# Performance work log

Hardware: AMD Instinct MI355X
Metric: run time of the kernel (lower is better)

The kernel has to match this reference:

```python
import jax, jax.numpy as jnp
import numpy as np

N = 100000
E = 1600000
IN_C = 128
HID = 32
HEADS = 4
OUT_C = 16
G = 128
NEG_SLOPE = 0.2


def setup_inputs() -> dict:
    key = jax.random.key(0)
    ks = jax.random.split(key, 16)
    x = jax.random.normal(ks[0], (N, IN_C), dtype=jnp.float32)
    edge_index = jax.random.randint(ks[1], (2, E), 0, N, dtype=jnp.int64)
    batch = jnp.sort(jax.random.randint(ks[2], (N,), 0, G, dtype=jnp.int64))
    node_weights = jax.random.uniform(ks[3], (N, 1), dtype=jnp.float32)
    s = 1.0 / np.sqrt(IN_C)
    W1 = jax.random.uniform(ks[4], (IN_C, HEADS * HID), jnp.float32, -s, s)
    att_src1 = jax.random.uniform(ks[5], (HEADS, HID), jnp.float32, -s, s)
    att_dst1 = jax.random.uniform(ks[6], (HEADS, HID), jnp.float32, -s, s)
    b1 = jnp.zeros((HEADS * HID,), jnp.float32)
    s2 = 1.0 / np.sqrt(HEADS * HID)
    W2 = jax.random.uniform(ks[7], (HEADS * HID, HID), jnp.float32, -s2, s2)
    att_src2 = jax.random.uniform(ks[8], (1, HID), jnp.float32, -s2, s2)
    att_dst2 = jax.random.uniform(ks[9], (1, HID), jnp.float32, -s2, s2)
    b2 = jnp.zeros((HID,), jnp.float32)
    s3 = 1.0 / np.sqrt(HID)
    fcW = jax.random.uniform(ks[10], (HID, OUT_C), jnp.float32, -s3, s3)
    fcb = jax.random.uniform(ks[11], (OUT_C,), jnp.float32, -s3, s3)
    return {"x": x, "edge_index": edge_index, "batch": batch,
            "node_weights": node_weights,
            "W1": W1, "att_src1": att_src1, "att_dst1": att_dst1, "b1": b1,
            "W2": W2, "att_src2": att_src2, "att_dst2": att_dst2, "b2": b2,
            "fcW": fcW, "fcb": fcb}


def gat_conv(x, src, dst, W, att_src, att_dst, bias, heads, ch, concat):
    n = x.shape[0]
    h = (x @ W).reshape(n, heads, ch)                       # [N,H,C]
    a_src = jnp.sum(h * att_src[None], axis=-1)             # [N,H]
    a_dst = jnp.sum(h * att_dst[None], axis=-1)             # [N,H]
    e = jax.nn.leaky_relu(a_src[src] + a_dst[dst], NEG_SLOPE)  # [E,H]
    # segment softmax over incoming edges of each destination node
    e_max = jax.ops.segment_max(e, dst, num_segments=n)
    ex = jnp.exp(e - e_max[dst])
    denom = jax.ops.segment_sum(ex, dst, num_segments=n)
    alpha = ex / denom[dst]                                 # [E,H]
    msg = h[src] * alpha[..., None]                         # [E,H,C]
    out = jax.ops.segment_sum(msg, dst, num_segments=n)     # [N,H,C]
    if concat:
        out = out.reshape(n, heads * ch)
    else:
        out = out.mean(axis=1)
    return out + bias


def reference(x, edge_index, batch, node_weights,
              W1, att_src1, att_dst1, b1,
              W2, att_src2, att_dst2, b2,
              fcW, fcb):
    n = x.shape[0]
    # PyG GATConv adds self-loops by default
    loop = jnp.arange(n, dtype=edge_index.dtype)
    src = jnp.concatenate([edge_index[0], loop])
    dst = jnp.concatenate([edge_index[1], loop])

    h = x * node_weights
    h = jax.nn.elu(gat_conv(h, src, dst, W1, att_src1, att_dst1, b1, HEADS, HID, True))
    h = jax.nn.elu(gat_conv(h, src, dst, W2, att_src2, att_dst2, b2, 1, HID, False))
    # global mean pool over graphs
    sums = jax.ops.segment_sum(h, batch, num_segments=G)
    cnts = jax.ops.segment_sum(jnp.ones((n,), h.dtype), batch, num_segments=G)
    pooled = sums / jnp.maximum(cnts, 1.0)[:, None]
    return pooled @ fcW + fcb
```

## Files before the change

### kernel.cpp

```cpp
#include <hip/hip_runtime.h>
#include <cstdint>

#define NGRAPH 128
#define NEG 0.2f
#define NB_MAX 512
#define BSH 8
#define BSZ 256
#define CAP 8192
#define RC  6144

typedef unsigned int uint;
typedef unsigned short ushort;
typedef unsigned char uchar;
typedef __attribute__((ext_vector_type(8))) short bf16x8;
typedef __attribute__((ext_vector_type(4))) float f32x4;
typedef __attribute__((ext_vector_type(2))) float f32x2;

union U4B { uint4 u; bf16x8 v; };

__device__ __forceinline__ ushort f2bf(float f) {
  uint u = __float_as_uint(f);
  uint r = (u + 0x7FFF + ((u >> 16) & 1)) >> 16;
  return (ushort)r;
}

__device__ __forceinline__ uint cvtpkbf16(float lo, float hi) {
  uint r;
  asm("v_cvt_pk_bf16_f32 %0, %1, %2" : "=v"(r) : "v"(lo), "v"(hi));
  return r;
}

__device__ __forceinline__ void pkfma(f32x2& acc, f32x2 f, f32x2 w) {
  asm("v_pk_fma_f32 %0, %1, %2, %0" : "+v"(acc) : "v"(f), "v"(w));
}

__device__ __forceinline__ float bperm_f(int addr, float v) {
  return __int_as_float(__builtin_amdgcn_ds_bpermute(addr, __float_as_int(v)));
}
__device__ __forceinline__ int bperm_i(int addr, int v) {
  return __builtin_amdgcn_ds_bpermute(addr, v);
}

__device__ __forceinline__ int wave_incl_scan_i(int v) {
  int lane = threadIdx.x & 63;
#pragma unroll
  for (int off = 1; off < 64; off <<= 1) {
    int u = __shfl_up(v, off, 64);
    if (lane >= off) v += u;
  }
  return v;
}

__global__ void k_bin(const int* __restrict__ ei,
                      const float* __restrict__ W1, const float* __restrict__ W2,
                      ushort* __restrict__ Wt1, ushort* __restrict__ Wt2,
                      int E, int Etot, int NB, int nbin,
                      int* __restrict__ bcur, uint* __restrict__ bbuf) {
  if (blockIdx.x >= (uint)nbin) {
    int t2 = (blockIdx.x - nbin) * 256 + threadIdx.x;
    if (t2 < 16384) {
      int n = t2 >> 7, k = t2 & 127;
      Wt1[t2] = f2bf(W1[k * 128 + n]);
    } else {
      int u = t2 - 16384;
      int n = u >> 7, k = u & 127;
      Wt2[u] = f2bf(W2[k * 32 + n]);
    }
    return;
  }
  __shared__ int h[NB_MAX];
  __shared__ int baseo[NB_MAX];
  __shared__ uint crec[4096];
  __shared__ ushort cbkt[4096];
  int t = threadIdx.x;
  for (int b = t; b < NB; b += 256) h[b] = 0;
  __syncthreads();
  int cbase = blockIdx.x * 4096;
  int cend = min(cbase + 4096, Etot);
  int nch = cend - cbase;
  for (int i = t; i < nch; i += 256) {
    int e = cbase + i;
    int s, d;
    if (e < E) { s = ei[e]; d = ei[E + e]; } else { s = e - E; d = s; }
    int b = d >> BSH;
    crec[i] = ((uint)(d & (BSZ - 1)) << 17) | (uint)s;
    cbkt[i] = (ushort)b;
    atomicAdd(&h[b], 1);
  }
  __syncthreads();
  for (int b = t; b < NB; b += 256) {
    int c = h[b];
    baseo[b] = c ? atomicAdd(&bcur[b], c) : 0;
    h[b] = 0;
  }
  __syncthreads();
  for (int i = t; i < nch; i += 256) {
    int b = cbkt[i];
    int r = atomicAdd(&h[b], 1);
    bbuf[(size_t)b * CAP + baseo[b] + r] = crec[i];
  }
}

__global__ void k_bg(const uint* __restrict__ bbuf, const int* __restrict__ bcur,
                     int NB, int N, int* __restrict__ offs, int* __restrict__ ssrc,
                     const float* __restrict__ x, const ushort* __restrict__ Wt,
                     const float* __restrict__ nw, const float* __restrict__ att_s,
                     const float* __restrict__ att_d, uchar* __restrict__ hb1,
                     float* __restrict__ asrc, float* __restrict__ adst) {
  __shared__ int sst[NB_MAX + 1];
  __shared__ int wsum2[4];
  __shared__ int deg[BSZ];
  __shared__ uint rcache[RC];
  if (blockIdx.x < (uint)NB) {
    int t = threadIdx.x, lane = t & 63, wid = t >> 6;
    int v0 = (2 * t < NB) ? bcur[2 * t] : 0;
    int v1 = (2 * t + 1 < NB) ? bcur[2 * t + 1] : 0;
    int s = v0 + v1;
    int sv = wave_incl_scan_i(s);
    if (lane == 63) wsum2[wid] = sv;
    deg[t] = 0;
    __syncthreads();
    if (t == 0) {
      int r = 0;
#pragma unroll
      for (int k = 0; k < 4; k++) { int x2 = wsum2[k]; wsum2[k] = r; r += x2; }
    }
    __syncthreads();
    int excl = wsum2[wid] + sv - s;
    sst[2 * t] = excl;
    sst[2 * t + 1] = excl + v0;
    if (t == 255) sst[512] = excl + v0 + v1;
    __syncthreads();
    int b = blockIdx.x;
    int ebeg = sst[b], eend = sst[b + 1];
    int cnt = eend - ebeg;
    const uint* brow = bbuf + (size_t)b * CAP;
    for (int i = t; i < cnt; i += BSZ) {
      uint rec = brow[i];
      if (i < RC) rcache[i] = rec;
      atomicAdd(&deg[rec >> 17], 1);
    }
    __syncthreads();
    int v = deg[t];
    int sv2 = wave_incl_scan_i(v);
    if (lane == 63) wsum2[wid] = sv2;
    __syncthreads();
    if (t == 0) {
      int r = 0;
#pragma unroll
      for (int k = 0; k < 4; k++) { int x2 = wsum2[k]; wsum2[k] = r; r += x2; }
    }
    __syncthreads();
    int excl2 = wsum2[wid] + sv2 - v;
    int node = (b << BSH) + t;
    if (node < N) offs[node] = ebeg + excl2;
    if (b == 0 && t == 0) offs[N] = sst[512];
    __syncthreads();
    deg[t] = excl2;
    __syncthreads();
    for (int i = t; i < cnt; i += BSZ) {
      uint rec = (i < RC) ? rcache[i] : brow[i];
      int r = atomicAdd(&deg[rec >> 17], 1);
      ssrc[ebeg + r] = (int)(rec & 0x1FFFF);
    }
    return;
  }
  int bid = blockIdx.x - NB;
  int wv = threadIdx.x >> 6, l = threadIdx.x & 63;
  int lg = l >> 4, lr = l & 15;
  int row0 = bid * 64 + wv * 16;
  int node = row0 + lr;
  bool valid = node < N;
  float sc = valid ? nw[node] : 0.f;
  bf16x8 xfr[4];
  const float* xr = x + (size_t)node * 128;
#pragma unroll
  for (int kc = 0; kc < 4; kc++) {
    float v[8];
    if (valid) {
      float4 q0 = *reinterpret_cast<const float4*>(xr + kc * 32 + lg * 8);
      float4 q1 = *reinterpret_cast<const float4*>(xr + kc * 32 + lg * 8 + 4);
      v[0] = q0.x; v[1] = q0.y; v[2] = q0.z; v[3] = q0.w;
      v[4] = q1.x; v[5] = q1.y; v[6] = q1.z; v[7] = q1.w;
    } else {
#pragma unroll
      for (int j = 0; j < 8; j++) v[j] = 0.f;
    }
    U4B a;
    a.u.x = cvtpkbf16(v[0] * sc, v[1] * sc);
    a.u.y = cvtpkbf16(v[2] * sc, v[3] * sc);
    a.u.z = cvtpkbf16(v[4] * sc, v[5] * sc);
    a.u.w = cvtpkbf16(v[6] * sc, v[7] * sc);
    xfr[kc] = a.v;
  }
  float pS[4] = {}, pD[4] = {};
#pragma unroll
  for (int ct = 0; ct < 8; ct++) {
    f32x4 acc = {0.f, 0.f, 0.f, 0.f};
    const ushort* wrow = Wt + (size_t)(ct * 16 + lr) * 128;
#pragma unroll
    for (int kc = 0; kc < 4; kc++) {
      U4B bfr;
      bfr.u = *reinterpret_cast<const uint4*>(wrow + kc * 32 + lg * 8);
      acc = __builtin_amdgcn_mfma_f32_16x16x32_bf16(bfr.v, xfr[kc], acc, 0, 0, 0);
    }
    int c0 = ct * 16 + lg * 4;
    if (valid) {
      uint u8 = (uint)__builtin_amdgcn_cvt_pk_fp8_f32(acc[0], acc[1], 0, false);
      u8 = (uint)__builtin_amdgcn_cvt_pk_fp8_f32(acc[2], acc[3], u8, true);
      *reinterpret_cast<uint*>(hb1 + (size_t)node * 128 + c0) = u8;
    }
    float4 as4 = *reinterpret_cast<const float4*>(att_s + c0);
    float4 ad4 = *reinterpret_cast<const float4*>(att_d + c0);
    int h = ct >> 1;
    pS[h] += acc[0] * as4.x + acc[1] * as4.y + acc[2] * as4.z + acc[3] * as4.w;
    pD[h] += acc[0] * ad4.x + acc[1] * ad4.y + acc[2] * ad4.z + acc[3] * ad4.w;
  }
#pragma unroll
  for (int off = 16; off < 64; off <<= 1) {
#pragma unroll
    for (int h = 0; h < 4; h++) {
      pS[h] += __shfl_xor(pS[h], off, 64);
      pD[h] += __shfl_xor(pD[h], off, 64);
    }
  }
  if (lg == 0 && valid) {
    *reinterpret_cast<float4*>(asrc + node * 4) = make_float4(pS[0], pS[1], pS[2], pS[3]);
    *reinterpret_cast<float4*>(adst + node * 4) = make_float4(pD[0], pD[1], pD[2], pD[3]);
  }
}

__global__ void k_aggr1(const int* __restrict__ offs, const int* __restrict__ ssrc,
                        const uchar* __restrict__ hb, const float* __restrict__ asrc,
                        const float* __restrict__ adst, const float* __restrict__ bias,
                        const ushort* __restrict__ Wt2, const float* __restrict__ as2,
                        const float* __restrict__ ad2, uchar* __restrict__ rec2,
                        float* __restrict__ adst2, int N) {
  __shared__ ushort rowl[4][136];
  int tid = threadIdx.x;
  int wv = tid >> 6, l = tid & 63;
  int d = blockIdx.x * 4 + wv;
  int dc = min(d, N - 1);
  int slot = l >> 3;
  int cb = l & 7;
  int h = cb >> 1;
  int hq = l & 3;
  int eidx = l >> 2;
  float adq = adst[dc * 4 + hq];
  int beg = offs[dc], end = offs[dc + 1];
  int endm1 = end - 1;
  const uchar* hbc = hb + cb * 16;
  int bp0 = (slot * 4 + h) << 2;
  int bp1 = bp0 + 128;
  f32x2 a2[8] = {};
  float dsp = 0.f;
  auto ACC = [&](uint4 p, float w) {
    f32x2 wp = {w, w};
    f32x2 f;
    f = __builtin_amdgcn_cvt_pk_f32_fp8(p.x, false); pkfma(a2[0], f, wp);
    f = __builtin_amdgcn_cvt_pk_f32_fp8(p.x, true);  pkfma(a2[1], f, wp);
    f = __builtin_amdgcn_cvt_pk_f32_fp8(p.y, false); pkfma(a2[2], f, wp);
    f = __builtin_amdgcn_cvt_pk_f32_fp8(p.y, true);  pkfma(a2[3], f, wp);
    f = __builtin_amdgcn_cvt_pk_f32_fp8(p.z, false); pkfma(a2[4], f, wp);
    f = __builtin_amdgcn_cvt_pk_f32_fp8(p.z, true);  pkfma(a2[5], f, wp);
    f = __builtin_amdgcn_cvt_pk_f32_fp8(p.w, false); pkfma(a2[6], f, wp);
    f = __builtin_amdgcn_cvt_pk_f32_fp8(p.w, true);  pkfma(a2[7], f, wp);
  };
  for (int base = beg; base < end; base += 32) {
    int eA = base + eidx;
    int eB = eA + 16;
    int sA = ssrc[min(eA, endm1)];
    int sB = ssrc[min(eB, endm1)];
    int s0 = bperm_i(bp0, sA);
    int s1 = bperm_i(bp1, sA);
    int s2 = bperm_i(bp0, sB);
    int s3 = bperm_i(bp1, sB);
    int rem = end - base;
    uint4 p0, p1, p2, p3;
    p0 = *reinterpret_cast<const uint4*>(hbc + (size_t)s0 * 128);
    if (rem > 8)  p1 = *reinterpret_cast<const uint4*>(hbc + (size_t)s1 * 128);
    if (rem > 16) p2 = *reinterpret_cast<const uint4*>(hbc + (size_t)s2 * 128);
    if (rem > 24) p3 = *reinterpret_cast<const uint4*>(hbc + (size_t)s3 * 128);
    float aA = asrc[sA * 4 + hq] + adq;
    float aB = asrc[sB * 4 + hq] + adq;
    aA = fmaxf(aA, aA * NEG);
    aB = fmaxf(aB, aB * NEG);
    float wA = (eA < end) ? __expf(aA) : 0.f;
    float wB = (eB < end) ? __expf(aB) : 0.f;
    dsp += wA + wB;
    float w0 = bperm_f(bp0, wA);
    float w1 = bperm_f(bp1, wA);
    float w2 = bperm_f(bp0, wB);
    float w3 = bperm_f(bp1, wB);
    ACC(p0, w0);
    if (rem > 8)  ACC(p1, w1);
    if (rem > 16) ACC(p2, w2);
    if (rem > 24) ACC(p3, w3);
  }
  dsp += __shfl_xor(dsp, 4, 64);
  dsp += __shfl_xor(dsp, 8, 64);
  dsp += __shfl_xor(dsp, 16, 64);
  dsp += __shfl_xor(dsp, 32, 64);
  float ds = bperm_f(h << 2, dsp);
  int b3 = (l >> 3) & 1, b4 = (l >> 4) & 1, b5 = (l >> 5) & 1;
  float t8[8];
#pragma unroll
  for (int r = 0; r < 8; r++) {
    float av = a2[r >> 1][r & 1];
    float bv = a2[(r + 8) >> 1][r & 1];
    float send = b3 ? av : bv;
    float recv = __shfl_xor(send, 8, 64);
    t8[r] = (b3 ? bv : av) + recv;
  }
  float t4[4];
#pragma unroll
  for (int r = 0; r < 4; r++) {
    float send = b4 ? t8[r] : t8[r + 4];
    float recv = __shfl_xor(send, 16, 64);
    t4[r] = (b4 ? t8[r + 4] : t8[r]) + recv;
  }
  float t2[2];
#pragma unroll
  for (int r = 0; r < 2; r++) {
    float send = b5 ? t4[r] : t4[r + 2];
    float recv = __shfl_xor(send, 32, 64);
    t2[r] = (b5 ? t4[r + 2] : t4[r]) + recv;
  }
  float inv = __builtin_amdgcn_rcpf(ds > 0.f ? ds : 1.f);
  int c0 = cb * 16 + b3 * 8 + b4 * 4 + b5 * 2;
  float2 bi = *reinterpret_cast<const float2*>(bias + c0);
  float r0 = fmaf(t2[0], inv, bi.x);
  float r1 = fmaf(t2[1], inv, bi.y);
  r0 = r0 > 0.f ? r0 : __expf(r0) - 1.f;
  r1 = r1 > 0.f ? r1 : __expf(r1) - 1.f;
  *reinterpret_cast<uint*>(&rowl[wv][c0]) = cvtpkbf16(r0, r1);
  __syncthreads();
  if (wv != 0) return;
  int lg = l >> 4, lr = l & 15;
  int rsel = lr & 3;
  bf16x8 bfrag[4];
#pragma unroll
  for (int kc = 0; kc < 4; kc++) {
    U4B bb;
    bb.u = *reinterpret_cast<const uint4*>(&rowl[rsel][kc * 32 + lg * 8]);
    bfrag[kc] = bb.v;
  }
  int dd = blockIdx.x * 4 + lr;
  bool vs = (lr < 4) && (dd < N);
  float pS = 0.f, pD = 0.f;
#pragma unroll
  for (int ct = 0; ct < 2; ct++) {
    f32x4 acc = {0.f, 0.f, 0.f, 0.f};
    const ushort* wrow = Wt2 + (size_t)(ct * 16 + lr) * 128;
#pragma unroll
    for (int kc = 0; kc < 4; kc++) {
      U4B bfr;
      bfr.u = *reinterpret_cast<const uint4*>(wrow + kc * 32 + lg * 8);
      acc = __builtin_amdgcn_mfma_f32_16x16x32_bf16(bfr.v, bfrag[kc], acc, 0, 0, 0);
    }
    int cg = ct * 16 + lg * 4;
    if (vs) {
      uint u8 = (uint)__builtin_amdgcn_cvt_pk_fp8_f32(acc[0], acc[1], 0, false);
      u8 = (uint)__builtin_amdgcn_cvt_pk_fp8_f32(acc[2], acc[3], u8, true);
      *reinterpret_cast<uint*>(rec2 + (size_t)dd * 64 + cg) = u8;
    }
    float4 as4 = *reinterpret_cast<const float4*>(as2 + cg);
    float4 ad4 = *reinterpret_cast<const float4*>(ad2 + cg);
    pS += acc[0] * as4.x + acc[1] * as4.y + acc[2] * as4.z + acc[3] * as4.w;
    pD += acc[0] * ad4.x + acc[1] * ad4.y + acc[2] * ad4.z + acc[3] * ad4.w;
  }
  pS += __shfl_xor(pS, 16, 64);
  pS += __shfl_xor(pS, 32, 64);
  pD += __shfl_xor(pD, 16, 64);
  pD += __shfl_xor(pD, 32, 64);
  if (vs && lg == 0) {
    *reinterpret_cast<float*>(rec2 + (size_t)dd * 64 + 32) = pS;
    adst2[dd] = pD;
  }
}

__global__ void k_aggr2(const int* __restrict__ offs, const int* __restrict__ ssrc,
                        const uchar* __restrict__ rec, const float* __restrict__ adst,
                        const float* __restrict__ bias, const int* __restrict__ batch,
                        float* __restrict__ gsum, int N) {
  __shared__ float sblk[4][32];
  int tid = threadIdx.x;
  int wid = tid >> 6, l = tid & 63;
  if (tid < 128) sblk[tid >> 5][tid & 31] = 0.f;
  __syncthreads();
  int d = blockIdx.x * 4 + wid;
  bool valid = d < N;
  int dc = valid ? d : N - 1;
  int slot = l >> 2;
  int k = l & 3;
  float ad = adst[dc];
  int beg = offs[dc];
  int end = valid ? offs[dc + 1] : beg;
  int endm1 = end - 1;
  const uchar* rk = rec + k * 8;
  int bq0 = slot << 2;
  int bq1 = (slot + 16) << 2;
  int bq2 = (slot + 32) << 2;
  int bq3 = (slot + 48) << 2;
  f32x2 a2[4] = {};
  float dsp = 0.f;
  auto ACC2 = [&](uint2 p, float w) {
    f32x2 wp = {w, w};
    f32x2 f;
    f = __builtin_amdgcn_cvt_pk_f32_fp8(p.x, false); pkfma(a2[0], f, wp);
    f = __builtin_amdgcn_cvt_pk_f32_fp8(p.x, true);  pkfma(a2[1], f, wp);
    f = __builtin_amdgcn_cvt_pk_f32_fp8(p.y, false); pkfma(a2[2], f, wp);
    f = __builtin_amdgcn_cvt_pk_f32_fp8(p.y, true);  pkfma(a2[3], f, wp);
  };
  for (int base = beg; base < end; base += 64) {
    int e = base + l;
    int sL = ssrc[min(e, endm1)];
    int s0 = bperm_i(bq0, sL);
    int s1 = bperm_i(bq1, sL);
    int s2 = bperm_i(bq2, sL);
    int s3 = bperm_i(bq3, sL);
    int rem = end - base;
    float av = *reinterpret_cast<const float*>(rec + (size_t)sL * 64 + 32);
    uint2 p0, p1, p2, p3;
    p0 = *reinterpret_cast<const uint2*>(rk + (size_t)s0 * 64);
    if (rem > 16) p1 = *reinterpret_cast<const uint2*>(rk + (size_t)s1 * 64);
    if (rem > 32) p2 = *reinterpret_cast<const uint2*>(rk + (size_t)s2 * 64);
    if (rem > 48) p3 = *reinterpret_cast<const uint2*>(rk + (size_t)s3 * 64);
    float xv = av + ad;
    xv = fmaxf(xv, xv * NEG);
    float wL = (e < end) ? __expf(xv) : 0.f;
    dsp += wL;
    float w0 = bperm_f(bq0, wL);
    float w1 = bperm_f(bq1, wL);
    float w2 = bperm_f(bq2, wL);
    float w3 = bperm_f(bq3, wL);
    ACC2(p0, w0);
    if (rem > 16) ACC2(p1, w1);
    if (rem > 32) ACC2(p2, w2);
    if (rem > 48) ACC2(p3, w3);
  }
  dsp += __shfl_xor(dsp, 1, 64);
  dsp += __shfl_xor(dsp, 2, 64);
  dsp += __shfl_xor(dsp, 4, 64);
  dsp += __shfl_xor(dsp, 8, 64);
  dsp += __shfl_xor(dsp, 16, 64);
  dsp += __shfl_xor(dsp, 32, 64);
  int b2 = (l >> 2) & 1, b3 = (l >> 3) & 1, b4 = (l >> 4) & 1;
  float t4[4];
#pragma unroll
  for (int r = 0; r < 4; r++) {
    float av = a2[r >> 1][r & 1];
    float bv = a2[(r + 4) >> 1][r & 1];
    float send = b2 ? av : bv;
    float recv = __shfl_xor(send, 4, 64);
    t4[r] = (b2 ? bv : av) + recv;
  }
  float t2[2];
#pragma unroll
  for (int r = 0; r < 2; r++) {
    float send = b3 ? t4[r] : t4[r + 2];
    float recv = __shfl_xor(send, 8, 64);
    t2[r] = (b3 ? t4[r + 2] : t4[r]) + recv;
  }
  float send = b4 ? t2[0] : t2[1];
  float recv = __shfl_xor(send, 16, 64);
  float t1 = (b4 ? t2[1] : t2[0]) + recv;
  t1 += __shfl_xor(t1, 32, 64);
  int gfirst = batch[blockIdx.x * 4];
  if (l < 32 && valid) {
    int c = k * 8 + b2 * 4 + b3 * 2 + b4;
    float inv = __builtin_amdgcn_rcpf(dsp > 0.f ? dsp : 1.f);
    float r = fmaf(t1, inv, bias[c]);
    r = r > 0.f ? r : __expf(r) - 1.f;
    int g = batch[dc];
    int sl = g - gfirst;
    if (sl < 4) atomicAdd(&sblk[sl][c], r);
    else atomicAdd(&gsum[g * 32 + c], r);
  }
  __syncthreads();
  if (tid < 128) {
    int sl = tid >> 5, c = tid & 31;
    float v = sblk[sl][c];
    int gg = gfirst + sl;
    if (v != 0.f && gg < NGRAPH) atomicAdd(&gsum[gg * 32 + c], v);
  }
}

__global__ void k_fc(const float* __restrict__ gsum, const int* __restrict__ batch,
                     const float* __restrict__ fcW, const float* __restrict__ fcb,
                     float* __restrict__ out, int N) {
  int g = blockIdx.x;
  int l = threadIdx.x;
  int lo = 0, hi = N;
  while (lo < hi) { int mid = (lo + hi) >> 1; if (batch[mid] < g) lo = mid + 1; else hi = mid; }
  int beg = lo;
  hi = N;
  while (lo < hi) { int mid = (lo + hi) >> 1; if (batch[mid] < g + 1) lo = mid + 1; else hi = mid; }
  int end = lo;
  float inv = 1.f / fmaxf((float)(end - beg), 1.f);
  __shared__ float pooled[32];
  if (l < 32) pooled[l] = gsum[g * 32 + l] * inv;
  __syncthreads();
  if (l < 16) {
    float r = fcb[l];
#pragma unroll
    for (int cc = 0; cc < 32; cc++) r += pooled[cc] * fcW[cc * 16 + l];
    out[g * 16 + l] = r;
  }
}

extern "C" void kernel_launch(void* const* d_in, const int* in_sizes, int n_in,
                              void* d_out, int out_size, void* d_ws, size_t ws_size,
                              hipStream_t stream) {
  const float* x     = (const float*)d_in[0];
  const int*   ei    = (const int*)d_in[1];
  const int*   batch = (const int*)d_in[2];
  const float* nw    = (const float*)d_in[3];
  const float* W1    = (const float*)d_in[4];
  const float* as1w  = (const float*)d_in[5];
  const float* ad1w  = (const float*)d_in[6];
  const float* b1    = (const float*)d_in[7];
  const float* W2    = (const float*)d_in[8];
  const float* as2w  = (const float*)d_in[9];
  const float* ad2w  = (const float*)d_in[10];
  const float* b2    = (const float*)d_in[11];
  const float* fcW   = (const float*)d_in[12];
  const float* fcb   = (const float*)d_in[13];
  float* out = (float*)d_out;

  const int N = in_sizes[0] / 128;
  const int E = in_sizes[1] / 2;
  const int Etot = E + N;
  const int NB = (N + BSZ - 1) >> BSH;

  char* w = (char*)d_ws;
  size_t ofs = 0;
  auto alloc = [&](size_t bytes) {
    char* p = w + ofs;
    ofs += (bytes + 255) & ~(size_t)255;
    return p;
  };
  uchar*  hb1    = (uchar*)alloc((size_t)N * 128);
  uchar*  rec2   = (uchar*)alloc((size_t)N * 64);
  float*  asrc1  = (float*)alloc((size_t)N * 4 * 4);
  float*  adst1  = (float*)alloc((size_t)N * 4 * 4);
  float*  adst2  = (float*)alloc((size_t)N * 4);
  ushort* Wt1    = (ushort*)alloc(16384 * 2);
  ushort* Wt2    = (ushort*)alloc(4096 * 2);
  int*    bcur   = (int*)alloc((size_t)NB * 4);
  float*  gsum   = (float*)alloc((size_t)NGRAPH * 32 * 4);
  int*    offs   = (int*)alloc((size_t)(N + 1) * 4);
  uint*   bbuf   = (uint*)alloc((size_t)NB * CAP * 4);
  int*    ssrc   = (int*)alloc((size_t)Etot * 4);

  size_t zlen = (size_t)((char*)gsum - (char*)bcur) + (size_t)NGRAPH * 32 * 4;
  hipMemsetAsync(bcur, 0, zlen, stream);

  const int nbin = (Etot + 4095) / 4096;
  k_bin<<<nbin + 80, 256, 0, stream>>>(ei, W1, W2, Wt1, Wt2, E, Etot, NB, nbin, bcur, bbuf);

  const int ngemm1 = (N + 63) / 64;
  k_bg<<<NB + ngemm1, 256, 0, stream>>>(bbuf, bcur, NB, N, offs, ssrc,
                                        x, Wt1, nw, as1w, ad1w, hb1, asrc1, adst1);

  k_aggr1<<<(N + 3) / 4, 256, 0, stream>>>(offs, ssrc, hb1, asrc1, adst1, b1,
                                           Wt2, as2w, ad2w, rec2, adst2, N);

  k_aggr2<<<(N + 3) / 4, 256, 0, stream>>>(offs, ssrc, rec2, adst2, b2, batch, gsum, N);

  k_fc<<<NGRAPH, 64, 0, stream>>>(gsum, batch, fcW, fcb, out, N);
}
```

Before: 295.4 us.

## Shrink binning chunk, drop LDS record cache, use nontemporal loads

Edge binning now uses 2048-edge chunks per block instead of 4096, so there are more blocks and each uses less shared memory. The bucket-sort kernel no longer caches records in LDS and re-reads them from global memory on the second pass, which frees about 24KB of LDS and should raise occupancy of the fused sort/GEMM kernel. Edge-index and x loads become nontemporal loads so these streaming reads do not pollute the cache. The trade-off is a second global read of the bucket records and more global atomic traffic on the bucket counters.

```diff
diff --git a/kernel.cpp b/kernel.cpp
--- a/kernel.cpp
+++ b/kernel.cpp
@@ -7,7 +7,7 @@
 #define BSH 8
 #define BSZ 256
 #define CAP 8192
-#define RC  6144
+#define CH  2048
 
 typedef unsigned int uint;
 typedef unsigned short ushort;
@@ -70,18 +70,21 @@
   }
   __shared__ int h[NB_MAX];
   __shared__ int baseo[NB_MAX];
-  __shared__ uint crec[4096];
-  __shared__ ushort cbkt[4096];
+  __shared__ uint crec[CH];
+  __shared__ ushort cbkt[CH];
   int t = threadIdx.x;
   for (int b = t; b < NB; b += 256) h[b] = 0;
   __syncthreads();
-  int cbase = blockIdx.x * 4096;
-  int cend = min(cbase + 4096, Etot);
+  int cbase = blockIdx.x * CH;
+  int cend = min(cbase + CH, Etot);
   int nch = cend - cbase;
   for (int i = t; i < nch; i += 256) {
     int e = cbase + i;
     int s, d;
-    if (e < E) { s = ei[e]; d = ei[E + e]; } else { s = e - E; d = s; }
+    if (e < E) {
+      s = __builtin_nontemporal_load(&ei[e]);
+      d = __builtin_nontemporal_load(&ei[E + e]);
+    } else { s = e - E; d = s; }
     int b = d >> BSH;
     crec[i] = ((uint)(d & (BSZ - 1)) << 17) | (uint)s;
     cbkt[i] = (ushort)b;
@@ -110,7 +113,6 @@
   __shared__ int sst[NB_MAX + 1];
   __shared__ int wsum2[4];
   __shared__ int deg[BSZ];
-  __shared__ uint rcache[RC];
   if (blockIdx.x < (uint)NB) {
     int t = threadIdx.x, lane = t & 63, wid = t >> 6;
     int v0 = (2 * t < NB) ? bcur[2 * t] : 0;
@@ -135,11 +137,8 @@
     int ebeg = sst[b], eend = sst[b + 1];
     int cnt = eend - ebeg;
     const uint* brow = bbuf + (size_t)b * CAP;
-    for (int i = t; i < cnt; i += BSZ) {
-      uint rec = brow[i];
-      if (i < RC) rcache[i] = rec;
-      atomicAdd(&deg[rec >> 17], 1);
-    }
+    for (int i = t; i < cnt; i += BSZ)
+      atomicAdd(&deg[brow[i] >> 17], 1);
     __syncthreads();
     int v = deg[t];
     int sv2 = wave_incl_scan_i(v);
@@ -159,7 +158,7 @@
     deg[t] = excl2;
     __syncthreads();
     for (int i = t; i < cnt; i += BSZ) {
-      uint rec = (i < RC) ? rcache[i] : brow[i];
+      uint rec = brow[i];
       int r = atomicAdd(&deg[rec >> 17], 1);
       ssrc[ebeg + r] = (int)(rec & 0x1FFFF);
     }
@@ -178,10 +177,10 @@
   for (int kc = 0; kc < 4; kc++) {
     float v[8];
     if (valid) {
-      float4 q0 = *reinterpret_cast<const float4*>(xr + kc * 32 + lg * 8);
-      float4 q1 = *reinterpret_cast<const float4*>(xr + kc * 32 + lg * 8 + 4);
-      v[0] = q0.x; v[1] = q0.y; v[2] = q0.z; v[3] = q0.w;
-      v[4] = q1.x; v[5] = q1.y; v[6] = q1.z; v[7] = q1.w;
+      f32x4 q0 = __builtin_nontemporal_load(reinterpret_cast<const f32x4*>(xr + kc * 32 + lg * 8));
+      f32x4 q1 = __builtin_nontemporal_load(reinterpret_cast<const f32x4*>(xr + kc * 32 + lg * 8 + 4));
+      v[0] = q0[0]; v[1] = q0[1]; v[2] = q0[2]; v[3] = q0[3];
+      v[4] = q1[0]; v[5] = q1[1]; v[6] = q1[2]; v[7] = q1[3];
     } else {
 #pragma unroll
       for (int j = 0; j < 8; j++) v[j] = 0.f;
@@ -556,7 +555,7 @@
   size_t zlen = (size_t)((char*)gsum - (char*)bcur) + (size_t)NGRAPH * 32 * 4;
   hipMemsetAsync(bcur, 0, zlen, stream);
 
-  const int nbin = (Etot + 4095) / 4096;
+  const int nbin = (Etot + CH - 1) / CH;
   k_bin<<<nbin + 80, 256, 0, stream>>>(ei, W1, W2, Wt1, Wt2, E, Etot, NB, nbin, bcur, bbuf);
 
   const int ngemm1 = (N + 63) / 64;
```

After: 305.7 us. +3.5%, slower.
